# Kernel tuning notes

Hardware: AMD Instinct MI355X
Metric: run time of the kernel (lower is better)

The kernel has to match this reference:

```python
import jax, jax.numpy as jnp
import numpy as np

N = 50000
E = 800000
G = 2500  # number of graphs


def setup_inputs() -> dict:
    key = jax.random.key(0)
    ks = jax.random.split(key, 10)
    x = jax.random.normal(ks[0], (N, 128), dtype=jnp.float32)
    edge_index = jax.random.randint(ks[1], (2, E), 0, N, dtype=jnp.int64)
    batch = jnp.sort(jax.random.randint(ks[2], (N,), 0, G, dtype=jnp.int64))
    def lin(k, fan_in, shape):
        return jax.random.normal(k, shape, dtype=jnp.float32) / np.sqrt(fan_in)
    return {
        'x': x, 'edge_index': edge_index, 'batch': batch,
        'W1': lin(ks[3], 128, (128, 64)), 'b1': jnp.zeros((64,), jnp.float32),
        'W2': lin(ks[4], 64, (64, 64)),  'b2': jnp.zeros((64,), jnp.float32),
        'W3': lin(ks[5], 64, (64, 64)),  'b3': jnp.zeros((64,), jnp.float32),
        'Wp1': lin(ks[6], 64, (64, 64)), 'bp1': jnp.zeros((64,), jnp.float32),
        'Wp2': lin(ks[7], 64, (64, 32)), 'bp2': jnp.zeros((32,), jnp.float32),
    }


def _gcn_norm(edge_index, n_nodes):
    # PyG GCNConv default: add self-loops, symmetric normalization
    loops = jnp.arange(n_nodes, dtype=edge_index.dtype)
    src = jnp.concatenate([edge_index[0], loops])
    dst = jnp.concatenate([edge_index[1], loops])
    deg = jax.ops.segment_sum(jnp.ones_like(dst, dtype=jnp.float32), dst,
                              num_segments=n_nodes)
    dis = jnp.where(deg > 0, jax.lax.rsqrt(deg), 0.0)
    norm = dis[src] * dis[dst]  # [E + N]
    return src, dst, norm


def _gcn_conv(x, W, b, src, dst, norm, n_nodes):
    h = x @ W                                   # transform first (small dim)
    m = h[src] * norm[:, None]                  # gather + scale
    out = jax.ops.segment_sum(m, dst, num_segments=n_nodes)  # scatter-add
    return out + b


def reference(x, edge_index, batch, W1, b1, W2, b2, W3, b3, Wp1, bp1, Wp2, bp2):
    n_nodes = x.shape[0]
    src, dst, norm = _gcn_norm(edge_index, n_nodes)
    x1 = jax.nn.relu(_gcn_conv(x, W1, b1, src, dst, norm, n_nodes))
    x2 = jax.nn.relu(_gcn_conv(x1, W2, b2, src, dst, norm, n_nodes))
    x3 = jax.nn.relu(_gcn_conv(x2, W3, b3, src, dst, norm, n_nodes))
    h = x1 + x2 + x3
    # global_mean_pool
    sums = jax.ops.segment_sum(h, batch, num_segments=G)
    counts = jax.ops.segment_sum(jnp.ones((n_nodes,), jnp.float32), batch,
                                 num_segments=G)
    pooled = sums / jnp.maximum(counts, 1.0)[:, None]
    z = jax.nn.relu(pooled @ Wp1 + bp1) @ Wp2 + bp2
    return z
```

## Files before the change

### kernel.cpp

```cpp
#include <hip/hip_runtime.h>
#include <math.h>


typedef short short8 __attribute__((ext_vector_type(8)));
typedef float f32x4 __attribute__((ext_vector_type(4)));

__device__ inline float bf2f(unsigned short h) {
    return __uint_as_float((unsigned)h << 16);
}
__device__ inline unsigned short f2bf(float f) {
    unsigned u = __float_as_uint(f);
    return (unsigned short)((u + (0x7FFFu + ((u >> 16) & 1u))) >> 16);
}
__device__ inline void bh8f(short8 u, float4& a, float4& b) {
    a.x = bf2f((unsigned short)u[0]); a.y = bf2f((unsigned short)u[1]);
    a.z = bf2f((unsigned short)u[2]); a.w = bf2f((unsigned short)u[3]);
    b.x = bf2f((unsigned short)u[4]); b.y = bf2f((unsigned short)u[5]);
    b.z = bf2f((unsigned short)u[6]); b.w = bf2f((unsigned short)u[7]);
}
__device__ inline float4 f4add(float4 a, float4 acc) {
    acc.x += a.x; acc.y += a.y; acc.z += a.z; acc.w += a.w;
    return acc;
}

template <int K>
__global__ __launch_bounds__(256) void k_hist_gemm(const int* __restrict__ dst,
                                                   int* __restrict__ hist, int E, int chunk,
                                                   const float* __restrict__ X,
                                                   const float* __restrict__ W,
                                                   unsigned short* __restrict__ H, int n) {
    __shared__ int hh[256];
    __shared__ short wt[64 * K];
    int t = threadIdx.x;
    if (blockIdx.x < 256) {
        hh[t] = 0;
        __syncthreads();
        int e0 = blockIdx.x * chunk;
        int e1 = min(e0 + chunk, E);
        for (int e = e0 + t; e < e1; e += 256) atomicAdd(&hh[dst[e] >> 8], 1);
        __syncthreads();
        hist[blockIdx.x * 256 + t] = hh[t];
        return;
    }
    for (int idx = t; idx < 64 * K; idx += 256) {
        int k = idx >> 6, ch = idx & 63;
        wt[ch * K + k] = (short)f2bf(W[idx]);
    }
    __syncthreads();
    int wave = t >> 6, lane = t & 63;
    int q = lane >> 4, l = lane & 15;
    int tile = (blockIdx.x - 256) * 4 + wave;
    if (tile * 16 >= n) return;
    int node = tile * 16 + l;
    short8 afr[4][K / 32];
#pragma unroll
    for (int mb = 0; mb < 4; mb++)
#pragma unroll
        for (int s = 0; s < K / 32; s++)
            afr[mb][s] = *(const short8*)(wt + (mb * 16 + l) * K + s * 32 + q * 8);
    f32x4 acc[4] = {};
    const float* xr = X + (size_t)node * K + q * 8;
#pragma unroll
    for (int s = 0; s < K / 32; s++) {
        float4 xa = *(const float4*)(xr + s * 32);
        float4 xb = *(const float4*)(xr + s * 32 + 4);
        short8 bfr;
        bfr[0] = (short)f2bf(xa.x); bfr[1] = (short)f2bf(xa.y);
        bfr[2] = (short)f2bf(xa.z); bfr[3] = (short)f2bf(xa.w);
        bfr[4] = (short)f2bf(xb.x); bfr[5] = (short)f2bf(xb.y);
        bfr[6] = (short)f2bf(xb.z); bfr[7] = (short)f2bf(xb.w);
#pragma unroll
        for (int mb = 0; mb < 4; mb++)
            acc[mb] = __builtin_amdgcn_mfma_f32_16x16x32_bf16(afr[mb][s], bfr, acc[mb], 0, 0, 0);
    }
#pragma unroll
    for (int mb = 0; mb < 4; mb++) {
        ushort4 u;
        u.x = f2bf(acc[mb][0]); u.y = f2bf(acc[mb][1]);
        u.z = f2bf(acc[mb][2]); u.w = f2bf(acc[mb][3]);
        ((ushort4*)H)[(size_t)node * 16 + mb * 4 + q] = u;
    }
}

__global__ void kA_colscan(const int* __restrict__ hist, int* __restrict__ cursorA,
                           int* __restrict__ tot) {
    __shared__ int s[256];
    int t = threadIdx.x;
    int k = blockIdx.x;
    int v = hist[t * 256 + k];
    s[t] = v;
    __syncthreads();
    for (int st = 1; st < 256; st <<= 1) {
        int u = s[t];
        if (t >= st) u += s[t - st];
        __syncthreads();
        s[t] = u;
        __syncthreads();
    }
    cursorA[t * 256 + k] = s[t] - v;
    if (t == 255) tot[k] = s[255];
}

__global__ void kA_scatter(const int* __restrict__ src, const int* __restrict__ dst,
                           const int* __restrict__ cursorA, const int* __restrict__ tot,
                           unsigned* __restrict__ ebuf, int E, int chunk) {
    __shared__ int s[256];
    __shared__ int cur[256];
    int t = threadIdx.x;
    s[t] = tot[t];
    __syncthreads();
    for (int st = 1; st < 256; st <<= 1) {
        int u = s[t];
        if (t >= st) u += s[t - st];
        __syncthreads();
        s[t] = u;
        __syncthreads();
    }
    int bstart = (t == 0) ? 0 : s[t - 1];
    cur[t] = cursorA[blockIdx.x * 256 + t] + bstart;
    __syncthreads();
    int e0 = blockIdx.x * chunk;
    int e1 = min(e0 + chunk, E);
    for (int e = e0 + t; e < e1; e += 256) {
        int d = dst[e];
        int p = atomicAdd(&cur[d >> 8], 1);
        ebuf[p] = ((unsigned)(d & 255) << 24) | (unsigned)src[e];
    }
}

__global__ void kB(const unsigned* __restrict__ ebuf, const int* __restrict__ tot,
                   float* __restrict__ dis, int* __restrict__ offsP,
                   unsigned* __restrict__ col, unsigned short* __restrict__ Hb,
                   unsigned short* __restrict__ Hb2, int N, int ZR) {
    __shared__ int s[256];
    __shared__ int h[256];
    __shared__ int cur[256];
    __shared__ float sdis[256];
    int t = threadIdx.x;
    int k = blockIdx.x;
    s[t] = tot[t];
    __syncthreads();
    for (int st = 1; st < 256; st <<= 1) {
        int u = s[t];
        if (t >= st) u += s[t - st];
        __syncthreads();
        s[t] = u;
        __syncthreads();
    }
    int lo = (k == 0) ? 0 : s[k - 1];
    int hi = s[k];
    int padbase = ((lo + 3) & ~3) + 768 * k;
    h[t] = 0;
    __syncthreads();
    for (int p = lo + t; p < hi; p += 256) atomicAdd(&h[ebuf[p] >> 24], 1);
    __syncthreads();
    int c = h[t];
    int cp = (c + 3) & ~3;
    int node = k * 256 + t;
    float dn = rsqrtf((float)(c + 1));
    sdis[t] = dn;
    if (node < N) dis[node] = dn;
    s[t] = cp;
    __syncthreads();
    for (int st = 1; st < 256; st <<= 1) {
        int u = s[t];
        if (t >= st) u += s[t - st];
        __syncthreads();
        s[t] = u;
        __syncthreads();
    }
    int start = padbase + s[t] - cp;
    if (node < N) offsP[node] = (start << 9) | cp;
    cur[t] = start;
    __syncthreads();
    for (int p = lo + t; p < hi; p += 256) {
        unsigned e = ebuf[p];
        int q = atomicAdd(&cur[e >> 24], 1);
        col[q] = e & 0x00FFFFFFu;
    }
    __syncthreads();
    if (node < N) {
        int end = start + cp;
        for (int q = cur[t]; q < end; q++) col[q] = (unsigned)ZR;
    }
    for (int idx = t; idx < 2048; idx += 256) {
        int nl = idx >> 3, cs = idx & 7;
        int nd = k * 256 + nl;
        if (nd >= N) continue;
        float d2 = sdis[nl];
        short8 v = ((const short8*)Hb)[(size_t)nd * 8 + cs];
        float4 a, b;
        bh8f(v, a, b);
        short8 o;
        o[0] = (short)f2bf(a.x * d2); o[1] = (short)f2bf(a.y * d2);
        o[2] = (short)f2bf(a.z * d2); o[3] = (short)f2bf(a.w * d2);
        o[4] = (short)f2bf(b.x * d2); o[5] = (short)f2bf(b.y * d2);
        o[6] = (short)f2bf(b.z * d2); o[7] = (short)f2bf(b.w * d2);
        ((short8*)Hb)[(size_t)nd * 8 + cs] = o;
    }
    if (k == 0) {
        if (t < 32) ((unsigned*)Hb)[(size_t)ZR * 32 + t] = 0u;
        else if (t < 64) ((unsigned*)Hb2)[(size_t)ZR * 32 + (t - 32)] = 0u;
    }
}

__global__ __launch_bounds__(256) void k_aggemm(const unsigned short* __restrict__ H,
                                                const unsigned* __restrict__ col,
                                                const int* __restrict__ offsP,
                                                const float* __restrict__ dis,
                                                const float* __restrict__ bias,
                                                const float* __restrict__ W,
                                                unsigned short* __restrict__ Xout,
                                                unsigned short* __restrict__ Hout, int n) {
    __shared__ short wt[64 * 64];
    __shared__ short vbuf[64 * 72];
    int t = threadIdx.x;
    for (int idx = t; idx < 64 * 64; idx += 256) {
        int k = idx >> 6, ch = idx & 63;
        wt[ch * 64 + k] = (short)f2bf(W[idx]);
    }
    const short8* Hs = (const short8*)H;
    int base = blockIdx.x * 64;
    int cs = t & 7;
    const float4* bias4 = (const float4*)bias;
    float4 bb0 = bias4[cs * 2];
    float4 bb1 = bias4[cs * 2 + 1];
#pragma unroll
    for (int r = 0; r < 2; r++) {
        int nl = r * 32 + (t >> 3);
        int node = base + nl;
        if (node < n) {
            float dn = dis[node];
            float4 acc0, acc1;
            bh8f(Hs[(size_t)node * 8 + cs], acc0, acc1);
            int po = offsP[node];
            int p = po >> 9, hi = p + (po & 511);
            for (; p < hi; p += 4) {
                uint4 e4 = *(const uint4*)(col + p);
                short8 g0 = Hs[(size_t)e4.x * 8 + cs];
                short8 g1 = Hs[(size_t)e4.y * 8 + cs];
                short8 g2 = Hs[(size_t)e4.z * 8 + cs];
                short8 g3 = Hs[(size_t)e4.w * 8 + cs];
                float4 a, b;
                bh8f(g0, a, b); acc0 = f4add(a, acc0); acc1 = f4add(b, acc1);
                bh8f(g1, a, b); acc0 = f4add(a, acc0); acc1 = f4add(b, acc1);
                bh8f(g2, a, b); acc0 = f4add(a, acc0); acc1 = f4add(b, acc1);
                bh8f(g3, a, b); acc0 = f4add(a, acc0); acc1 = f4add(b, acc1);
            }
            float4 v0, v1;
            v0.x = fmaxf(acc0.x * dn + bb0.x, 0.f);
            v0.y = fmaxf(acc0.y * dn + bb0.y, 0.f);
            v0.z = fmaxf(acc0.z * dn + bb0.z, 0.f);
            v0.w = fmaxf(acc0.w * dn + bb0.w, 0.f);
            v1.x = fmaxf(acc1.x * dn + bb1.x, 0.f);
            v1.y = fmaxf(acc1.y * dn + bb1.y, 0.f);
            v1.z = fmaxf(acc1.z * dn + bb1.z, 0.f);
            v1.w = fmaxf(acc1.w * dn + bb1.w, 0.f);
            short8 o;
            o[0] = (short)f2bf(v0.x); o[1] = (short)f2bf(v0.y);
            o[2] = (short)f2bf(v0.z); o[3] = (short)f2bf(v0.w);
            o[4] = (short)f2bf(v1.x); o[5] = (short)f2bf(v1.y);
            o[6] = (short)f2bf(v1.z); o[7] = (short)f2bf(v1.w);
            ((short8*)Xout)[(size_t)node * 8 + cs] = o;
            *(short8*)(vbuf + nl * 72 + cs * 8) = o;
        }
    }
    __syncthreads();
    int wave = t >> 6, lane = t & 63;
    int q = lane >> 4, l = lane & 15;
    if (base + wave * 16 >= n) return;
    int node = base + wave * 16 + l;
    float dn2 = dis[node];
    short8 afr[4][2];
#pragma unroll
    for (int mb = 0; mb < 4; mb++)
#pragma unroll
        for (int s = 0; s < 2; s++)
            afr[mb][s] = *(const short8*)(wt + (mb * 16 + l) * 64 + s * 32 + q * 8);
    f32x4 acc[4] = {};
#pragma unroll
    for (int s = 0; s < 2; s++) {
        short8 bfr = *(const short8*)(vbuf + (wave * 16 + l) * 72 + s * 32 + q * 8);
#pragma unroll
        for (int mb = 0; mb < 4; mb++)
            acc[mb] = __builtin_amdgcn_mfma_f32_16x16x32_bf16(afr[mb][s], bfr, acc[mb], 0, 0, 0);
    }
#pragma unroll
    for (int mb = 0; mb < 4; mb++) {
        ushort4 u;
        u.x = f2bf(acc[mb][0] * dn2); u.y = f2bf(acc[mb][1] * dn2);
        u.z = f2bf(acc[mb][2] * dn2); u.w = f2bf(acc[mb][3] * dn2);
        ((ushort4*)Hout)[(size_t)node * 16 + mb * 4 + q] = u;
    }
}

__global__ void k_agg3(const unsigned short* __restrict__ H, const unsigned* __restrict__ col,
                       const int* __restrict__ offsP, const float* __restrict__ dis,
                       const float* __restrict__ bias,
                       const unsigned short* __restrict__ add1,
                       const unsigned short* __restrict__ add2,
                       float* __restrict__ OutS, int n) {
    int t = threadIdx.x;
    int node = blockIdx.x * 32 + (t >> 3);
    if (node >= n) return;
    int lane = t & 7;
    const short8* Hs = (const short8*)H;
    float dn = dis[node];
    float4 acc0, acc1;
    bh8f(Hs[(size_t)node * 8 + lane], acc0, acc1);
    int po = offsP[node];
    int p = po >> 9, hi = p + (po & 511);
    for (; p < hi; p += 4) {
        uint4 e4 = *(const uint4*)(col + p);
        short8 g0 = Hs[(size_t)e4.x * 8 + lane];
        short8 g1 = Hs[(size_t)e4.y * 8 + lane];
        short8 g2 = Hs[(size_t)e4.z * 8 + lane];
        short8 g3 = Hs[(size_t)e4.w * 8 + lane];
        float4 a, b;
        bh8f(g0, a, b); acc0 = f4add(a, acc0); acc1 = f4add(b, acc1);
        bh8f(g1, a, b); acc0 = f4add(a, acc0); acc1 = f4add(b, acc1);
        bh8f(g2, a, b); acc0 = f4add(a, acc0); acc1 = f4add(b, acc1);
        bh8f(g3, a, b); acc0 = f4add(a, acc0); acc1 = f4add(b, acc1);
    }
    const float4* bias4 = (const float4*)bias;
    float4 bb0 = bias4[lane * 2];
    float4 bb1 = bias4[lane * 2 + 1];
    float4 v0, v1;
    v0.x = fmaxf(acc0.x * dn + bb0.x, 0.f);
    v0.y = fmaxf(acc0.y * dn + bb0.y, 0.f);
    v0.z = fmaxf(acc0.z * dn + bb0.z, 0.f);
    v0.w = fmaxf(acc0.w * dn + bb0.w, 0.f);
    v1.x = fmaxf(acc1.x * dn + bb1.x, 0.f);
    v1.y = fmaxf(acc1.y * dn + bb1.y, 0.f);
    v1.z = fmaxf(acc1.z * dn + bb1.z, 0.f);
    v1.w = fmaxf(acc1.w * dn + bb1.w, 0.f);
    size_t slot = (size_t)node * 8 + lane;
    float4 a10, a11, a20, a21;
    bh8f(((const short8*)add1)[slot], a10, a11);
    bh8f(((const short8*)add2)[slot], a20, a21);
    v0.x += a10.x + a20.x; v0.y += a10.y + a20.y;
    v0.z += a10.z + a20.z; v0.w += a10.w + a20.w;
    v1.x += a11.x + a21.x; v1.y += a11.y + a21.y;
    v1.z += a11.z + a21.z; v1.w += a11.w + a21.w;
    float4* S4 = (float4*)OutS;
    size_t oi = (size_t)node * 16 + (size_t)lane * 2;
    S4[oi] = v0;
    S4[oi + 1] = v1;
}

__global__ void k_poolhead(const float* __restrict__ S, const int* __restrict__ batch,
                           const float* __restrict__ Wp1, const float* __restrict__ bp1,
                           const float* __restrict__ Wp2, const float* __restrict__ bp2,
                           float* __restrict__ out, int n, int G) {
    int g = blockIdx.x;
    int j = threadIdx.x;
    int a = 0, b = n;
    while (a < b) { int m = (a + b) >> 1; if (batch[m] < g) a = m + 1; else b = m; }
    int beg = a;
    b = n;
    while (a < b) { int m = (a + b) >> 1; if (batch[m] < g + 1) a = m + 1; else b = m; }
    int end = a;
    float sum = 0.f;
    int i = beg;
    for (; i + 2 <= end; i += 2)
        sum += S[(size_t)i * 64 + j] + S[(size_t)(i + 1) * 64 + j];
    if (i < end) sum += S[(size_t)i * 64 + j];
    float cnt = (float)(end - beg);
    float p = sum / fmaxf(cnt, 1.f);
    __shared__ float ps[64];
    __shared__ float ts[64];
    ps[j] = p;
    __syncthreads();
    float t1 = bp1[j];
#pragma unroll 8
    for (int k = 0; k < 64; k++) t1 += ps[k] * Wp1[k * 64 + j];
    t1 = fmaxf(t1, 0.f);
    ts[j] = t1;
    __syncthreads();
    if (j < 32) {
        float o = bp2[j];
#pragma unroll 8
        for (int k = 0; k < 64; k++) o += ts[k] * Wp2[k * 32 + j];
        out[(size_t)g * 32 + j] = o;
    }
}

extern "C" void kernel_launch(void* const* d_in, const int* in_sizes, int n_in,
                              void* d_out, int out_size, void* d_ws, size_t ws_size,
                              hipStream_t stream) {
    const float* x   = (const float*)d_in[0];
    const int*   ei  = (const int*)d_in[1];
    const int*   bat = (const int*)d_in[2];
    const float* W1  = (const float*)d_in[3];
    const float* b1  = (const float*)d_in[4];
    const float* W2  = (const float*)d_in[5];
    const float* b2  = (const float*)d_in[6];
    const float* W3  = (const float*)d_in[7];
    const float* b3  = (const float*)d_in[8];
    const float* Wp1 = (const float*)d_in[9];
    const float* bp1 = (const float*)d_in[10];
    const float* Wp2 = (const float*)d_in[11];
    const float* bp2 = (const float*)d_in[12];

    int N = in_sizes[0] / 128;
    int E = in_sizes[1] / 2;
    int G = out_size / 32;
    const int* src = ei;
    const int* dst = ei + E;

    char* w = (char*)d_ws;
    auto alloc = [&](size_t bytes) -> void* {
        void* p = (void*)w;
        w += (bytes + 255) & ~(size_t)255;
        return p;
    };
    int NB = (N + 255) / 256;
    int ZR = N;
    int*            offsP   = (int*)alloc((size_t)N * 4);
    unsigned*       col     = (unsigned*)alloc(((size_t)E + 3 * (size_t)N + 2048) * 4);
    float*          dis     = (float*)alloc((size_t)N * 4);
    int*            hist    = (int*)alloc((size_t)256 * 256 * 4);
    int*            cursorA = (int*)alloc((size_t)256 * 256 * 4);
    int*            tot     = (int*)alloc((size_t)256 * 4);
    unsigned*       ebuf    = (unsigned*)alloc((size_t)E * 4);
    unsigned short* Hb      = (unsigned short*)alloc(((size_t)N + 16) * 64 * 2);
    unsigned short* Hb2     = (unsigned short*)alloc(((size_t)N + 16) * 64 * 2);
    unsigned short* X1      = (unsigned short*)alloc((size_t)N * 64 * 2);
    unsigned short* X2      = (unsigned short*)alloc((size_t)N * 64 * 2);
    float*          S       = (float*)alloc((size_t)N * 64 * 4);

    int chunk = (E + 255) / 256;
    int ggemm = ((N >> 4) + 3) / 4;
    int gfuse = (N + 63) / 64;
    int gagg  = (N + 31) / 32;

    k_hist_gemm<128><<<256 + ggemm, 256, 0, stream>>>(dst, hist, E, chunk, x, W1, Hb, N);
    kA_colscan<<<256, 256, 0, stream>>>(hist, cursorA, tot);
    kA_scatter<<<256, 256, 0, stream>>>(src, dst, cursorA, tot, ebuf, E, chunk);
    kB<<<NB, 256, 0, stream>>>(ebuf, tot, dis, offsP, col, Hb, Hb2, N, ZR);

    k_aggemm<<<gfuse, 256, 0, stream>>>(Hb, col, offsP, dis, b1, W2, X1, Hb2, N);
    k_aggemm<<<gfuse, 256, 0, stream>>>(Hb2, col, offsP, dis, b2, W3, X2, Hb, N);
    k_agg3<<<gagg, 256, 0, stream>>>(Hb, col, offsP, dis, b3, X1, X2, S, N);

    k_poolhead<<<G, 64, 0, stream>>>(S, bat, Wp1, bp1, Wp2, bp2, (float*)d_out, N, G);
}
```

Before: 216.9 us.

## Sort nodes by degree within blocks and unroll gather loop by eight

kB now builds a per-256-node permutation that orders nodes by descending padded degree, using a 128-bin counting sort in shared memory. The aggregation kernels process nodes through this permutation, so the 8 threads and the warps that share a wavefront handle nodes of similar degree, which reduces divergence from uneven neighbour counts. The gather loop is also unrolled to 8 edges per iteration with a 4-edge tail, to keep more loads in flight. The cost is an extra indirection load per node and scattered output writes, since node order no longer follows memory order.

Measured after the change: 221.2 us. No clear change (+2.0%).

```diff
diff --git a/kernel.cpp b/kernel.cpp
--- a/kernel.cpp
+++ b/kernel.cpp
@@ -131,14 +131,18 @@
 __global__ void kB(const unsigned* __restrict__ ebuf, const int* __restrict__ tot,
                    float* __restrict__ dis, int* __restrict__ offsP,
                    unsigned* __restrict__ col, unsigned short* __restrict__ Hb,
-                   unsigned short* __restrict__ Hb2, int N, int ZR) {
+                   unsigned short* __restrict__ Hb2, int* __restrict__ perm,
+                   int N, int ZR) {
     __shared__ int s[256];
     __shared__ int h[256];
     __shared__ int cur[256];
     __shared__ float sdis[256];
+    __shared__ int lh[128];
+    __shared__ int ls[128];
     int t = threadIdx.x;
     int k = blockIdx.x;
     s[t] = tot[t];
+    if (t < 128) lh[t] = 0;
     __syncthreads();
     for (int st = 1; st < 256; st <<= 1) {
         int u = s[t];
@@ -160,6 +164,11 @@
     float dn = rsqrtf((float)(c + 1));
     sdis[t] = dn;
     if (node < N) dis[node] = dn;
+    int bin = cp >> 2;
+    if (bin > 127) bin = 127;
+    bin = 127 - bin;
+    int rk = 0;
+    if (node < N) rk = atomicAdd(&lh[bin], 1);
     s[t] = cp;
     __syncthreads();
     for (int st = 1; st < 256; st <<= 1) {
@@ -172,7 +181,16 @@
     int start = padbase + s[t] - cp;
     if (node < N) offsP[node] = (start << 9) | cp;
     cur[t] = start;
-    __syncthreads();
+    if (t < 128) ls[t] = lh[t];
+    __syncthreads();
+    for (int st = 1; st < 128; st <<= 1) {
+        int u = 0;
+        if (t < 128) { u = ls[t]; if (t >= st) u += ls[t - st]; }
+        __syncthreads();
+        if (t < 128) ls[t] = u;
+        __syncthreads();
+    }
+    if (node < N) perm[k * 256 + ls[bin] - lh[bin] + rk] = node;
     for (int p = lo + t; p < hi; p += 256) {
         unsigned e = ebuf[p];
         int q = atomicAdd(&cur[e >> 24], 1);
@@ -210,6 +228,7 @@
                                                 const float* __restrict__ dis,
                                                 const float* __restrict__ bias,
                                                 const float* __restrict__ W,
+                                                const int* __restrict__ perm,
                                                 unsigned short* __restrict__ Xout,
                                                 unsigned short* __restrict__ Hout, int n) {
     __shared__ short wt[64 * 64];
@@ -228,14 +247,36 @@
 #pragma unroll
     for (int r = 0; r < 2; r++) {
         int nl = r * 32 + (t >> 3);
-        int node = base + nl;
-        if (node < n) {
+        int slot = base + nl;
+        if (slot < n) {
+            int node = perm[slot];
             float dn = dis[node];
             float4 acc0, acc1;
             bh8f(Hs[(size_t)node * 8 + cs], acc0, acc1);
             int po = offsP[node];
-            int p = po >> 9, hi = p + (po & 511);
-            for (; p < hi; p += 4) {
+            int p = po >> 9, hiP = p + (po & 511);
+            for (; p + 8 <= hiP; p += 8) {
+                uint4 ea = *(const uint4*)(col + p);
+                uint4 eb = *(const uint4*)(col + p + 4);
+                short8 g0 = Hs[(size_t)ea.x * 8 + cs];
+                short8 g1 = Hs[(size_t)ea.y * 8 + cs];
+                short8 g2 = Hs[(size_t)ea.z * 8 + cs];
+                short8 g3 = Hs[(size_t)ea.w * 8 + cs];
+                short8 g4 = Hs[(size_t)eb.x * 8 + cs];
+                short8 g5 = Hs[(size_t)eb.y * 8 + cs];
+                short8 g6 = Hs[(size_t)eb.z * 8 + cs];
+                short8 g7 = Hs[(size_t)eb.w * 8 + cs];
+                float4 a, b;
+                bh8f(g0, a, b); acc0 = f4add(a, acc0); acc1 = f4add(b, acc1);
+                bh8f(g1, a, b); acc0 = f4add(a, acc0); acc1 = f4add(b, acc1);
+                bh8f(g2, a, b); acc0 = f4add(a, acc0); acc1 = f4add(b, acc1);
+                bh8f(g3, a, b); acc0 = f4add(a, acc0); acc1 = f4add(b, acc1);
+                bh8f(g4, a, b); acc0 = f4add(a, acc0); acc1 = f4add(b, acc1);
+                bh8f(g5, a, b); acc0 = f4add(a, acc0); acc1 = f4add(b, acc1);
+                bh8f(g6, a, b); acc0 = f4add(a, acc0); acc1 = f4add(b, acc1);
+                bh8f(g7, a, b); acc0 = f4add(a, acc0); acc1 = f4add(b, acc1);
+            }
+            if (p < hiP) {
                 uint4 e4 = *(const uint4*)(col + p);
                 short8 g0 = Hs[(size_t)e4.x * 8 + cs];
                 short8 g1 = Hs[(size_t)e4.y * 8 + cs];
@@ -269,7 +310,7 @@
     int wave = t >> 6, lane = t & 63;
     int q = lane >> 4, l = lane & 15;
     if (base + wave * 16 >= n) return;
-    int node = base + wave * 16 + l;
+    int node = perm[base + wave * 16 + l];
     float dn2 = dis[node];
     short8 afr[4][2];
 #pragma unroll
@@ -299,18 +340,41 @@
                        const float* __restrict__ bias,
                        const unsigned short* __restrict__ add1,
                        const unsigned short* __restrict__ add2,
+                       const int* __restrict__ perm,
                        float* __restrict__ OutS, int n) {
     int t = threadIdx.x;
-    int node = blockIdx.x * 32 + (t >> 3);
-    if (node >= n) return;
+    int slot = blockIdx.x * 32 + (t >> 3);
+    if (slot >= n) return;
+    int node = perm[slot];
     int lane = t & 7;
     const short8* Hs = (const short8*)H;
     float dn = dis[node];
     float4 acc0, acc1;
     bh8f(Hs[(size_t)node * 8 + lane], acc0, acc1);
     int po = offsP[node];
-    int p = po >> 9, hi = p + (po & 511);
-    for (; p < hi; p += 4) {
+    int p = po >> 9, hiP = p + (po & 511);
+    for (; p + 8 <= hiP; p += 8) {
+        uint4 ea = *(const uint4*)(col + p);
+        uint4 eb = *(const uint4*)(col + p + 4);
+        short8 g0 = Hs[(size_t)ea.x * 8 + lane];
+        short8 g1 = Hs[(size_t)ea.y * 8 + lane];
+        short8 g2 = Hs[(size_t)ea.z * 8 + lane];
+        short8 g3 = Hs[(size_t)ea.w * 8 + lane];
+        short8 g4 = Hs[(size_t)eb.x * 8 + lane];
+        short8 g5 = Hs[(size_t)eb.y * 8 + lane];
+        short8 g6 = Hs[(size_t)eb.z * 8 + lane];
+        short8 g7 = Hs[(size_t)eb.w * 8 + lane];
+        float4 a, b;
+        bh8f(g0, a, b); acc0 = f4add(a, acc0); acc1 = f4add(b, acc1);
+        bh8f(g1, a, b); acc0 = f4add(a, acc0); acc1 = f4add(b, acc1);
+        bh8f(g2, a, b); acc0 = f4add(a, acc0); acc1 = f4add(b, acc1);
+        bh8f(g3, a, b); acc0 = f4add(a, acc0); acc1 = f4add(b, acc1);
+        bh8f(g4, a, b); acc0 = f4add(a, acc0); acc1 = f4add(b, acc1);
+        bh8f(g5, a, b); acc0 = f4add(a, acc0); acc1 = f4add(b, acc1);
+        bh8f(g6, a, b); acc0 = f4add(a, acc0); acc1 = f4add(b, acc1);
+        bh8f(g7, a, b); acc0 = f4add(a, acc0); acc1 = f4add(b, acc1);
+    }
+    if (p < hiP) {
         uint4 e4 = *(const uint4*)(col + p);
         short8 g0 = Hs[(size_t)e4.x * 8 + lane];
         short8 g1 = Hs[(size_t)e4.y * 8 + lane];
@@ -334,10 +398,10 @@
     v1.y = fmaxf(acc1.y * dn + bb1.y, 0.f);
     v1.z = fmaxf(acc1.z * dn + bb1.z, 0.f);
     v1.w = fmaxf(acc1.w * dn + bb1.w, 0.f);
-    size_t slot = (size_t)node * 8 + lane;
+    size_t slotR = (size_t)node * 8 + lane;
     float4 a10, a11, a20, a21;
-    bh8f(((const short8*)add1)[slot], a10, a11);
-    bh8f(((const short8*)add2)[slot], a20, a21);
+    bh8f(((const short8*)add1)[slotR], a10, a11);
+    bh8f(((const short8*)add2)[slotR], a20, a21);
     v0.x += a10.x + a20.x; v0.y += a10.y + a20.y;
     v0.z += a10.z + a20.z; v0.w += a10.w + a20.w;
     v1.x += a11.x + a21.x; v1.y += a11.y + a21.y;
@@ -423,6 +487,7 @@
     int*            cursorA = (int*)alloc((size_t)256 * 256 * 4);
     int*            tot     = (int*)alloc((size_t)256 * 4);
     unsigned*       ebuf    = (unsigned*)alloc((size_t)E * 4);
+    int*            perm    = (int*)alloc((size_t)(NB * 256) * 4);
     unsigned short* Hb      = (unsigned short*)alloc(((size_t)N + 16) * 64 * 2);
     unsigned short* Hb2     = (unsigned short*)alloc(((size_t)N + 16) * 64 * 2);
     unsigned short* X1      = (unsigned short*)alloc((size_t)N * 64 * 2);
@@ -437,11 +502,11 @@
     k_hist_gemm<128><<<256 + ggemm, 256, 0, stream>>>(dst, hist, E, chunk, x, W1, Hb, N);
     kA_colscan<<<256, 256, 0, stream>>>(hist, cursorA, tot);
     kA_scatter<<<256, 256, 0, stream>>>(src, dst, cursorA, tot, ebuf, E, chunk);
-    kB<<<NB, 256, 0, stream>>>(ebuf, tot, dis, offsP, col, Hb, Hb2, N, ZR);
-
-    k_aggemm<<<gfuse, 256, 0, stream>>>(Hb, col, offsP, dis, b1, W2, X1, Hb2, N);
-    k_aggemm<<<gfuse, 256, 0, stream>>>(Hb2, col, offsP, dis, b2, W3, X2, Hb, N);
-    k_agg3<<<gagg, 256, 0, stream>>>(Hb, col, offsP, dis, b3, X1, X2, S, N);
+    kB<<<NB, 256, 0, stream>>>(ebuf, tot, dis, offsP, col, Hb, Hb2, perm, N, ZR);
+
+    k_aggemm<<<gfuse, 256, 0, stream>>>(Hb, col, offsP, dis, b1, W2, perm, X1, Hb2, N);
+    k_aggemm<<<gfuse, 256, 0, stream>>>(Hb2, col, offsP, dis, b2, W3, perm, X2, Hb, N);
+    k_agg3<<<gagg, 256, 0, stream>>>(Hb, col, offsP, dis, b3, X1, X2, perm, S, N);
 
     k_poolhead<<<G, 64, 0, stream>>>(S, bat, Wp1, bp1, Wp2, bp2, (float*)d_out, N, G);
 }
```
